# Kernel tuning notes

Hardware: AMD Instinct MI355X
Metric: run time of the kernel (lower is better)

## Reference

```python
import jax, jax.numpy as jnp
import numpy as np

NEG_INF = -1.0e9  # matches torch code's masked fill value


def setup_inputs() -> dict:
    key = jax.random.key(0)
    k1, k2, k3, k4 = jax.random.split(key, 4)
    n, q, s, d, v = 8, 4096, 4096, 64, 64
    return {
        "queries_nqd": jax.random.normal(k1, (n, q, d), dtype=jnp.float32),
        "keys_nsd": jax.random.normal(k2, (n, s, d), dtype=jnp.float32),
        "values_nsv": jax.random.normal(k3, (n, s, v), dtype=jnp.float32),
        "attention_mask_nqs": jax.random.randint(k4, (n, q, s), 0, 2).astype(jnp.bool_),
    }


def reference(queries_nqd, keys_nsd, values_nsv, attention_mask_nqs):
    d = queries_nqd.shape[-1]
    scale = 1.0 / jnp.sqrt(jnp.asarray(d, dtype=queries_nqd.dtype))
    # [n,q,s] = [n,q,d] @ [n,d,s]
    scores_nqs = jnp.einsum("nqd,nsd->nqs", queries_nqd, keys_nsd) * scale
    scores_nqs = jnp.where(attention_mask_nqs, scores_nqs, jnp.asarray(NEG_INF, scores_nqs.dtype))
    probs_nqs = jax.nn.softmax(scores_nqs, axis=-1)
    # dropout p=0.0 (eval) -> identity
    return jnp.einsum("nqs,nsv->nqv", probs_nqs, values_nsv)
```

## Files before the change

### kernel.cpp

```cpp
#include <hip/hip_runtime.h>
#include <hip/hip_bf16.h>


#define NHEADS 8
#define QLEN   4096
#define SLEN   4096
#define DDIM   64
#define VDIM   64
#define SBLK   64
#define QBLK   64
#define NWAVES 4
#define NCHUNK (SLEN / SBLK)

typedef __bf16          bf16x4 __attribute__((ext_vector_type(4)));
typedef __bf16          bf16x8 __attribute__((ext_vector_type(8)));
typedef float           f32x4  __attribute__((ext_vector_type(4)));
typedef unsigned int    u32x4  __attribute__((ext_vector_type(4)));
typedef unsigned short  u16x4  __attribute__((ext_vector_type(4)));

#define KSWZ(s) (((s) & 7) << 4)
#define VSWZ(v) ((((v) >> 2) & 7) << 4)

__device__ __forceinline__ int detect_mfmt(const unsigned char* __restrict__ M) {
  const int lane = threadIdx.x & 63;
  u32x4 w = *((const u32x4*)M + lane);
  unsigned o = w[0] | w[1] | w[2] | w[3];
  unsigned comb = ((o & 0x00FFFF00u) ? 1u : 0u) | ((o & 0x000000FFu) ? 2u : 0u);
  comb |= __shfl_xor((int)comb, 1);  comb |= __shfl_xor((int)comb, 2);
  comb |= __shfl_xor((int)comb, 4);  comb |= __shfl_xor((int)comb, 8);
  comb |= __shfl_xor((int)comb, 16); comb |= __shfl_xor((int)comb, 32);
  return ((comb & 1u) == 0u) ? 1 : (((comb & 2u) == 0u) ? 2 : 0);
}

struct MaskRegs {
  unsigned w8[4];
  u32x4    w32[4];
};

__global__ __launch_bounds__(256, 2)
void attn_fwd_kernel(const float* __restrict__ Qg, const float* __restrict__ Kg,
                     const float* __restrict__ Vg, const unsigned char* __restrict__ Mg,
                     float* __restrict__ Og)
{
  __shared__ __align__(16) unsigned short Ksh[2][64 * 64];
  __shared__ __align__(16) unsigned short Vsh[2][64 * 64];
  __shared__ __align__(16) unsigned short Psh[NWAVES][16 * 64];

  const int mfmt = detect_mfmt(Mg);

  const int tid  = threadIdx.x;
  const int wave = tid >> 6;
  const int lane = tid & 63;
  const int g    = lane >> 4;
  const int lq   = lane & 15;

  const int head = blockIdx.x;
  const int qblk = blockIdx.y;

  const float* Qp = Qg + ((size_t)head * QLEN + (size_t)qblk * QBLK) * DDIM;
  const float* Kp = Kg + (size_t)head * SLEN * DDIM;
  const float* Vp = Vg + (size_t)head * SLEN * VDIM;
  float* Op = Og + ((size_t)head * QLEN + (size_t)qblk * QBLK) * DDIM;

  const float QSCALE = 0.125f * 1.44269504f;
  const int qrow = wave * 16 + lq;
  bf16x8 qf[2];
#pragma unroll
  for (int ks = 0; ks < 2; ++ks) {
    const float* qp = Qp + (size_t)qrow * DDIM + 8 * g + 32 * ks;
    f32x4 a = *(const f32x4*)qp;
    f32x4 b = *(const f32x4*)(qp + 4);
    bf16x8 t;
#pragma unroll
    for (int j = 0; j < 4; ++j) { t[j] = (__bf16)(a[j] * QSCALE); t[4 + j] = (__bf16)(b[j] * QSCALE); }
    qf[ks] = t;
  }

  const size_t mrow_elems = ((size_t)head * QLEN + (size_t)qblk * QBLK + qrow) * SLEN;
  const unsigned char* mrow8  = Mg + mrow_elems;
  const unsigned*      mrow32 = (const unsigned*)Mg + mrow_elems;

  f32x4 oacc[4];
#pragma unroll
  for (int vt = 0; vt < 4; ++vt) oacc[vt] = (f32x4){0.f, 0.f, 0.f, 0.f};
  float m_run = -INFINITY;
  float l_run = 0.f;

#define PREFETCH_KV(S0)                                                        \
  _Pragma("unroll")                                                            \
  for (int it = 0; it < 4; ++it) {                                             \
    int srow = (tid >> 4) + it * 16;                                           \
    int d0   = (tid & 15) * 4;                                                 \
    kpre[it] = *(const f32x4*)(Kp + (size_t)((S0) + srow) * DDIM + d0);        \
    vpre[it] = *(const f32x4*)(Vp + (size_t)((S0) + srow) * VDIM + d0);        \
  }

#define WRITE_KV(BUF)                                                          \
  _Pragma("unroll")                                                            \
  for (int it = 0; it < 4; ++it) {                                             \
    int srow = (tid >> 4) + it * 16;                                           \
    int d0   = (tid & 15) * 4;                                                 \
    bf16x4 kb;                                                                 \
    _Pragma("unroll") for (int j = 0; j < 4; ++j) kb[j] = (__bf16)kpre[it][j]; \
    int koff = (srow * 128 + d0 * 2) ^ KSWZ(srow);                             \
    *(u16x4*)((char*)Ksh[BUF] + koff) = __builtin_bit_cast(u16x4, kb);         \
    _Pragma("unroll")                                                          \
    for (int j = 0; j < 4; ++j) {                                              \
      int v = d0 + j;                                                          \
      unsigned short b = __builtin_bit_cast(unsigned short, (__bf16)vpre[it][j]); \
      int voff = (v * 128 + srow * 2) ^ VSWZ(v);                               \
      *(unsigned short*)((char*)Vsh[BUF] + voff) = b;                          \
    }                                                                          \
  }

#define LOAD_MASK(MR, S0)                                                      \
  if (mfmt == 0) {                                                             \
    _Pragma("unroll")                                                          \
    for (int st = 0; st < 4; ++st)                                             \
      MR.w8[st] = *(const unsigned*)(mrow8 + (S0) + 16 * st + 4 * g);          \
  } else {                                                                     \
    _Pragma("unroll")                                                          \
    for (int st = 0; st < 4; ++st)                                             \
      MR.w32[st] = *(const u32x4*)(mrow32 + (S0) + 16 * st + 4 * g);           \
  }

#define CHUNK_BODY(C, CUR, MUSE, MLOAD) {                                      \
  const bool hasn = ((C) + 1 < NCHUNK);                                        \
  f32x4 kpre[4]; f32x4 vpre[4];                                                \
  if (hasn) {                                                                  \
    const int s0n = ((C) + 1) * SBLK;                                          \
    PREFETCH_KV(s0n);                                                          \
    LOAD_MASK(MLOAD, s0n);                                                     \
  }                                                                            \
                               \
  f32x4 sacc[4];                                                               \
  _Pragma("unroll")                                                            \
  for (int st = 0; st < 4; ++st) sacc[st] = (f32x4){0.f, 0.f, 0.f, 0.f};       \
  _Pragma("unroll")                                                            \
  for (int st = 0; st < 4; ++st) {                                             \
    int srow = lq + 16 * st;                                                   \
    _Pragma("unroll")                                                          \
    for (int ks = 0; ks < 2; ++ks) {                                           \
      int off = (srow * 128 + (8 * g + 32 * ks) * 2) ^ KSWZ(srow);             \
      bf16x8 kf = *(const bf16x8*)((const char*)Ksh[CUR] + off);               \
      sacc[st] = __builtin_amdgcn_mfma_f32_16x16x32_bf16(kf, qf[ks], sacc[st], 0, 0, 0); \
    }                                                                          \
  }                                                                            \
                      \
  float vals[4][4];                                                            \
  float mloc = -INFINITY;                                                      \
  _Pragma("unroll")                                                            \
  for (int st = 0; st < 4; ++st) {                                             \
    bool keep[4];                                                              \
    if (mfmt == 0) {                                                           \
      _Pragma("unroll")                                                        \
      for (int r = 0; r < 4; ++r) keep[r] = ((MUSE.w8[st] >> (8 * r)) & 0xFFu) != 0u; \
    } else {                                                                   \
      _Pragma("unroll")                                                        \
      for (int r = 0; r < 4; ++r) keep[r] = MUSE.w32[st][r] != 0u;             \
    }                                                                          \
    _Pragma("unroll")                                                          \
    for (int r = 0; r < 4; ++r) {                                              \
      float v = keep[r] ? sacc[st][r] : -1.0e9f;                               \
      vals[st][r] = v;                                                         \
      mloc = fmaxf(mloc, v);                                                   \
    }                                                                          \
  }                                                                            \
  mloc = fmaxf(mloc, __shfl_xor(mloc, 16));                                    \
  mloc = fmaxf(mloc, __shfl_xor(mloc, 32));                                    \
  float m_new = fmaxf(m_run, mloc);                                            \
  float alpha = __builtin_amdgcn_exp2f(m_run - m_new);                         \
  float lsum = 0.f;                                                            \
  _Pragma("unroll")                                                            \
  for (int st = 0; st < 4; ++st) {                                             \
    bf16x4 pb;                                                                 \
    _Pragma("unroll")                                                          \
    for (int r = 0; r < 4; ++r) {                                              \
      float p = __builtin_amdgcn_exp2f(vals[st][r] - m_new);                   \
      lsum += p;                                                               \
      pb[r] = (__bf16)p;                                                       \
    }                                                                          \
    int off = (lq * 128 + (16 * st + 4 * g) * 2) ^ KSWZ(lq);                   \
    *(u16x4*)((char*)Psh[wave] + off) = __builtin_bit_cast(u16x4, pb);         \
  }                                                                            \
  lsum += __shfl_xor(lsum, 16);                                                \
  lsum += __shfl_xor(lsum, 32);                                                \
  l_run = l_run * alpha + lsum;                                                \
  m_run = m_new;                                                               \
  _Pragma("unroll")                                                            \
  for (int vt = 0; vt < 4; ++vt) {                                             \
    _Pragma("unroll")                                                          \
    for (int r = 0; r < 4; ++r) oacc[vt][r] *= alpha;                          \
  }                                                                            \
                                                \
  _Pragma("unroll")                                                            \
  for (int ks = 0; ks < 2; ++ks) {                                             \
    int poff = (lq * 128 + (8 * g + 32 * ks) * 2) ^ KSWZ(lq);                  \
    bf16x8 pf = *(const bf16x8*)((const char*)Psh[wave] + poff);               \
    _Pragma("unroll")                                                          \
    for (int vt = 0; vt < 4; ++vt) {                                           \
      int vrow = lq + 16 * vt;                                                 \
      int voff = (vrow * 128 + (8 * g + 32 * ks) * 2) ^ VSWZ(vrow);            \
      bf16x8 vf = *(const bf16x8*)((const char*)Vsh[CUR] + voff);              \
      oacc[vt] = __builtin_amdgcn_mfma_f32_16x16x32_bf16(vf, pf, oacc[vt], 0, 0, 0); \
    }                                                                          \
  }                                                                            \
  if (hasn) { WRITE_KV((CUR) ^ 1); }                                           \
  __syncthreads();                                                             \
}

  MaskRegs mA, mB;

  {
    f32x4 kpre[4]; f32x4 vpre[4];
    PREFETCH_KV(0);
    LOAD_MASK(mA, 0);
    WRITE_KV(0);
    __syncthreads();
  }

  for (int cc = 0; cc < NCHUNK; cc += 2) {
    CHUNK_BODY(cc,     0, mA, mB);
    CHUNK_BODY(cc + 1, 1, mB, mA);
  }

  float inv_l = 1.0f / l_run;
  float* orow = Op + (size_t)qrow * VDIM;
#pragma unroll
  for (int vt = 0; vt < 4; ++vt) {
    f32x4 o;
#pragma unroll
    for (int r = 0; r < 4; ++r) o[r] = oacc[vt][r] * inv_l;
    *(f32x4*)(orow + 16 * vt + 4 * g) = o;
  }
}

extern "C" void kernel_launch(void* const* d_in, const int* in_sizes, int n_in,
                              void* d_out, int out_size, void* d_ws, size_t ws_size,
                              hipStream_t stream) {
  const float* Qg = (const float*)d_in[0];
  const float* Kg = (const float*)d_in[1];
  const float* Vg = (const float*)d_in[2];
  const unsigned char* Mg = (const unsigned char*)d_in[3];
  float* Og = (float*)d_out;

  dim3 grid(NHEADS, QLEN / QBLK);
  dim3 block(256);
  attn_fwd_kernel<<<grid, block, 0, stream>>>(Qg, Kg, Vg, Mg, Og);
}
```

Before: 155.2 us.

## Double Q tile, deepen K/V/mask prefetch, lazy rescale, template mask format

Moves to 128-query blocks with 8 waves, so each K/V tile staged in shared memory serves twice as many queries. Prefetch now runs two chunks ahead in register buffers. The mask format check becomes a template parameter with two launches, where the non-matching kernel exits early. It also adds a lazy online-softmax rescale that skips the alpha correction when the new max stays within 8 (log2 units), plus s_setprio around the MFMA sections. The cost is more registers at 512 threads, an extra kernel launch, and a grid half the previous size.

```diff
diff --git a/kernel.cpp b/kernel.cpp
--- a/kernel.cpp
+++ b/kernel.cpp
@@ -8,8 +8,8 @@
 #define DDIM   64
 #define VDIM   64
 #define SBLK   64
-#define QBLK   64
-#define NWAVES 4
+#define QBLK   128
+#define NWAVES 8
 #define NCHUNK (SLEN / SBLK)
 
 typedef __bf16          bf16x4 __attribute__((ext_vector_type(4)));
@@ -20,6 +20,7 @@
 
 #define KSWZ(s) (((s) & 7) << 4)
 #define VSWZ(v) ((((v) >> 2) & 7) << 4)
+#define CLAMPC(c) ((c) < NCHUNK ? (c) : NCHUNK - 1)
 
 __device__ __forceinline__ int detect_mfmt(const unsigned char* __restrict__ M) {
   const int lane = threadIdx.x & 63;
@@ -32,21 +33,20 @@
   return ((comb & 1u) == 0u) ? 1 : (((comb & 2u) == 0u) ? 2 : 0);
 }
 
-struct MaskRegs {
-  unsigned w8[4];
-  u32x4    w32[4];
-};
-
-__global__ __launch_bounds__(256, 2)
-void attn_fwd_kernel(const float* __restrict__ Qg, const float* __restrict__ Kg,
-                     const float* __restrict__ Vg, const unsigned char* __restrict__ Mg,
-                     float* __restrict__ Og)
+template<bool U8>
+__global__ __launch_bounds__(512, 2)
+void attn_fwd(const float* __restrict__ Qg, const float* __restrict__ Kg,
+              const float* __restrict__ Vg, const unsigned char* __restrict__ Mg,
+              float* __restrict__ Og)
 {
   __shared__ __align__(16) unsigned short Ksh[2][64 * 64];
   __shared__ __align__(16) unsigned short Vsh[2][64 * 64];
   __shared__ __align__(16) unsigned short Psh[NWAVES][16 * 64];
 
-  const int mfmt = detect_mfmt(Mg);
+  {
+    const int mfmt = detect_mfmt(Mg);
+    if (U8 ? (mfmt != 0) : (mfmt == 0)) return;
+  }
 
   const int tid  = threadIdx.x;
   const int wave = tid >> 6;
@@ -86,56 +86,56 @@
   float m_run = -INFINITY;
   float l_run = 0.f;
 
-#define PREFETCH_KV(S0)                                                        \
-  _Pragma("unroll")                                                            \
-  for (int it = 0; it < 4; ++it) {                                             \
-    int srow = (tid >> 4) + it * 16;                                           \
+  f32x4 kpA[2], vpA[2], kpB[2], vpB[2];
+  unsigned m8A[4],  m8B[4];
+  u32x4    m32A[4], m32B[4];
+
+#define PREFETCH_KV(C, KP, VP)                                                 \
+  _Pragma("unroll")                                                            \
+  for (int it = 0; it < 2; ++it) {                                             \
+    int srow = (tid >> 4) + it * 32;                                           \
     int d0   = (tid & 15) * 4;                                                 \
-    kpre[it] = *(const f32x4*)(Kp + (size_t)((S0) + srow) * DDIM + d0);        \
-    vpre[it] = *(const f32x4*)(Vp + (size_t)((S0) + srow) * VDIM + d0);        \
-  }
-
-#define WRITE_KV(BUF)                                                          \
-  _Pragma("unroll")                                                            \
-  for (int it = 0; it < 4; ++it) {                                             \
-    int srow = (tid >> 4) + it * 16;                                           \
+    size_t gs = (size_t)(CLAMPC(C) * SBLK + srow);                             \
+    KP[it] = *(const f32x4*)(Kp + gs * DDIM + d0);                             \
+    VP[it] = *(const f32x4*)(Vp + gs * VDIM + d0);                             \
+  }
+
+#define WRITE_KV(BUF, KP, VP)                                                  \
+  _Pragma("unroll")                                                            \
+  for (int it = 0; it < 2; ++it) {                                             \
+    int srow = (tid >> 4) + it * 32;                                           \
     int d0   = (tid & 15) * 4;                                                 \
     bf16x4 kb;                                                                 \
-    _Pragma("unroll") for (int j = 0; j < 4; ++j) kb[j] = (__bf16)kpre[it][j]; \
+    _Pragma("unroll") for (int j = 0; j < 4; ++j) kb[j] = (__bf16)KP[it][j];   \
     int koff = (srow * 128 + d0 * 2) ^ KSWZ(srow);                             \
     *(u16x4*)((char*)Ksh[BUF] + koff) = __builtin_bit_cast(u16x4, kb);         \
     _Pragma("unroll")                                                          \
     for (int j = 0; j < 4; ++j) {                                              \
       int v = d0 + j;                                                          \
-      unsigned short b = __builtin_bit_cast(unsigned short, (__bf16)vpre[it][j]); \
+      unsigned short b = __builtin_bit_cast(unsigned short, (__bf16)VP[it][j]); \
       int voff = (v * 128 + srow * 2) ^ VSWZ(v);                               \
       *(unsigned short*)((char*)Vsh[BUF] + voff) = b;                          \
     }                                                                          \
   }
 
-#define LOAD_MASK(MR, S0)                                                      \
-  if (mfmt == 0) {                                                             \
+#define LOAD_MASK(M8, M32, C)                                                  \
+  if constexpr (U8) {                                                          \
     _Pragma("unroll")                                                          \
     for (int st = 0; st < 4; ++st)                                             \
-      MR.w8[st] = *(const unsigned*)(mrow8 + (S0) + 16 * st + 4 * g);          \
+      M8[st] = *(const unsigned*)(mrow8 + (size_t)CLAMPC(C) * SBLK + 16 * st + 4 * g); \
   } else {                                                                     \
     _Pragma("unroll")                                                          \
     for (int st = 0; st < 4; ++st)                                             \
-      MR.w32[st] = *(const u32x4*)(mrow32 + (S0) + 16 * st + 4 * g);           \
-  }
-
-#define CHUNK_BODY(C, CUR, MUSE, MLOAD) {                                      \
-  const bool hasn = ((C) + 1 < NCHUNK);                                        \
-  f32x4 kpre[4]; f32x4 vpre[4];                                                \
-  if (hasn) {                                                                  \
-    const int s0n = ((C) + 1) * SBLK;                                          \
-    PREFETCH_KV(s0n);                                                          \
-    LOAD_MASK(MLOAD, s0n);                                                     \
-  }                                                                            \
+      M32[st] = *(const u32x4*)(mrow32 + (size_t)CLAMPC(C) * SBLK + 16 * st + 4 * g); \
+  }
+
+#define CHUNK_BODY(C, CUR, KPF, VPF, KPW, VPW, M8U, M32U) {                    \
+  PREFETCH_KV((C) + 2, KPF, VPF);                                              \
                                \
   f32x4 sacc[4];                                                               \
   _Pragma("unroll")                                                            \
   for (int st = 0; st < 4; ++st) sacc[st] = (f32x4){0.f, 0.f, 0.f, 0.f};       \
+  __builtin_amdgcn_s_setprio(1);                                               \
   _Pragma("unroll")                                                            \
   for (int st = 0; st < 4; ++st) {                                             \
     int srow = lq + 16 * st;                                                   \
@@ -146,18 +146,19 @@
       sacc[st] = __builtin_amdgcn_mfma_f32_16x16x32_bf16(kf, qf[ks], sacc[st], 0, 0, 0); \
     }                                                                          \
   }                                                                            \
+  __builtin_amdgcn_s_setprio(0);                                               \
                       \
   float vals[4][4];                                                            \
   float mloc = -INFINITY;                                                      \
   _Pragma("unroll")                                                            \
   for (int st = 0; st < 4; ++st) {                                             \
     bool keep[4];                                                              \
-    if (mfmt == 0) {                                                           \
+    if constexpr (U8) {                                                        \
       _Pragma("unroll")                                                        \
-      for (int r = 0; r < 4; ++r) keep[r] = ((MUSE.w8[st] >> (8 * r)) & 0xFFu) != 0u; \
+      for (int r = 0; r < 4; ++r) keep[r] = ((M8U[st] >> (8 * r)) & 0xFFu) != 0u; \
     } else {                                                                   \
       _Pragma("unroll")                                                        \
-      for (int r = 0; r < 4; ++r) keep[r] = MUSE.w32[st][r] != 0u;             \
+      for (int r = 0; r < 4; ++r) keep[r] = M32U[st][r] != 0u;                 \
     }                                                                          \
     _Pragma("unroll")                                                          \
     for (int r = 0; r < 4; ++r) {                                              \
@@ -166,17 +167,28 @@
       mloc = fmaxf(mloc, v);                                                   \
     }                                                                          \
   }                                                                            \
+  LOAD_MASK(M8U, M32U, (C) + 2);            \
   mloc = fmaxf(mloc, __shfl_xor(mloc, 16));                                    \
   mloc = fmaxf(mloc, __shfl_xor(mloc, 32));                                    \
-  float m_new = fmaxf(m_run, mloc);                                            \
-  float alpha = __builtin_amdgcn_exp2f(m_run - m_new);                         \
+      \
+  if (!__all(mloc <= m_run + 8.0f)) {                                          \
+    float m_new = fmaxf(m_run, mloc);                                          \
+    float alpha = __builtin_amdgcn_exp2f(m_run - m_new);                       \
+    l_run *= alpha;                                                            \
+    _Pragma("unroll")                                                          \
+    for (int vt = 0; vt < 4; ++vt) {                                           \
+      _Pragma("unroll")                                                        \
+      for (int r = 0; r < 4; ++r) oacc[vt][r] *= alpha;                        \
+    }                                                                          \
+    m_run = m_new;                                                             \
+  }                                                                            \
   float lsum = 0.f;                                                            \
   _Pragma("unroll")                                                            \
   for (int st = 0; st < 4; ++st) {                                             \
     bf16x4 pb;                                                                 \
     _Pragma("unroll")                                                          \
     for (int r = 0; r < 4; ++r) {                                              \
-      float p = __builtin_amdgcn_exp2f(vals[st][r] - m_new);                   \
+      float p = __builtin_amdgcn_exp2f(vals[st][r] - m_run);                   \
       lsum += p;                                                               \
       pb[r] = (__bf16)p;                                                       \
     }                                                                          \
@@ -185,14 +197,9 @@
   }                                                                            \
   lsum += __shfl_xor(lsum, 16);                                                \
   lsum += __shfl_xor(lsum, 32);                                                \
-  l_run = l_run * alpha + lsum;                                                \
-  m_run = m_new;                                                               \
-  _Pragma("unroll")                                                            \
-  for (int vt = 0; vt < 4; ++vt) {                                             \
-    _Pragma("unroll")                                                          \
-    for (int r = 0; r < 4; ++r) oacc[vt][r] *= alpha;                          \
-  }                                                                            \
+  l_run += lsum;                                                               \
                                                 \
+  __builtin_amdgcn_s_setprio(1);                                               \
   _Pragma("unroll")                                                            \
   for (int ks = 0; ks < 2; ++ks) {                                             \
     int poff = (lq * 128 + (8 * g + 32 * ks) * 2) ^ KSWZ(lq);                  \
@@ -205,23 +212,21 @@
       oacc[vt] = __builtin_amdgcn_mfma_f32_16x16x32_bf16(vf, pf, oacc[vt], 0, 0, 0); \
     }                                                                          \
   }                                                                            \
-  if (hasn) { WRITE_KV((CUR) ^ 1); }                                           \
+  __builtin_amdgcn_s_setprio(0);                                               \
+  WRITE_KV((CUR) ^ 1, KPW, VPW);         \
   __syncthreads();                                                             \
 }
 
-  MaskRegs mA, mB;
-
-  {
-    f32x4 kpre[4]; f32x4 vpre[4];
-    PREFETCH_KV(0);
-    LOAD_MASK(mA, 0);
-    WRITE_KV(0);
-    __syncthreads();
-  }
+  PREFETCH_KV(0, kpA, vpA);
+  LOAD_MASK(m8A, m32A, 0);
+  PREFETCH_KV(1, kpB, vpB);
+  LOAD_MASK(m8B, m32B, 1);
+  WRITE_KV(0, kpA, vpA);
+  __syncthreads();
 
   for (int cc = 0; cc < NCHUNK; cc += 2) {
-    CHUNK_BODY(cc,     0, mA, mB);
-    CHUNK_BODY(cc + 1, 1, mB, mA);
+    CHUNK_BODY(cc,     0, kpA, vpA, kpB, vpB, m8A, m32A);
+    CHUNK_BODY(cc + 1, 1, kpB, vpB, kpA, vpA, m8B, m32B);
   }
 
   float inv_l = 1.0f / l_run;
@@ -233,6 +238,10 @@
     for (int r = 0; r < 4; ++r) o[r] = oacc[vt][r] * inv_l;
     *(f32x4*)(orow + 16 * vt + 4 * g) = o;
   }
+#undef PREFETCH_KV
+#undef WRITE_KV
+#undef LOAD_MASK
+#undef CHUNK_BODY
 }
 
 extern "C" void kernel_launch(void* const* d_in, const int* in_sizes, int n_in,
@@ -245,6 +254,7 @@
   float* Og = (float*)d_out;
 
   dim3 grid(NHEADS, QLEN / QBLK);
-  dim3 block(256);
-  attn_fwd_kernel<<<grid, block, 0, stream>>>(Qg, Kg, Vg, Mg, Og);
-}
+  dim3 block(512);
+  attn_fwd<true ><<<grid, block, 0, stream>>>(Qg, Kg, Vg, Mg, Og);
+  attn_fwd<false><<<grid, block, 0, stream>>>(Qg, Kg, Vg, Mg, Og);
+}
```

After: 148.0 us. -4.6%, faster.
